# Optimization experiments

Measured on AMD Instinct MI355X. Metric: run time of the kernel, lower is better.

## Reference

```python
import jax, jax.numpy as jnp
import numpy as np

B, S, T = 64, 64, 64          # batch, encoder seq len, decoder context_length
V, D, H, L = 32000, 512, 1024, 256  # vocab, embed, hidden, latent


def _gru_cell(x, h, W_ih, W_hh, b_ih, b_hh):
    # PyTorch GRUCell math. x:[B,D_in], h:[B,H]
    gi = x @ W_ih.T + b_ih            # [B,3H]
    gh = h @ W_hh.T + b_hh            # [B,3H]
    i_r, i_z, i_n = jnp.split(gi, 3, axis=-1)
    h_r, h_z, h_n = jnp.split(gh, 3, axis=-1)
    r = jax.nn.sigmoid(i_r + h_r)
    z = jax.nn.sigmoid(i_z + h_z)
    n = jnp.tanh(i_n + r * h_n)
    return (1.0 - z) * n + z * h


def setup_inputs() -> dict:
    key = jax.random.key(0)
    ks = jax.random.split(key, 16)
    s = 0.02
    inp = {
        "x": jax.random.randint(ks[0], (B, S), 0, V),
        "eps": jax.random.normal(ks[1], (B, L), dtype=jnp.float32),
        "E": jax.random.normal(ks[2], (V, D), dtype=jnp.float32) * s,
        # encoder GRU
        "W_ih_enc": jax.random.normal(ks[3], (3 * H, D), dtype=jnp.float32) * s,
        "W_hh_enc": jax.random.normal(ks[4], (3 * H, H), dtype=jnp.float32) * s,
        "b_ih_enc": jnp.zeros((3 * H,), jnp.float32),
        "b_hh_enc": jnp.zeros((3 * H,), jnp.float32),
        # latent heads
        "W_mu": jax.random.normal(ks[5], (L, H), dtype=jnp.float32) * s,
        "b_mu": jnp.zeros((L,), jnp.float32),
        "W_lv": jax.random.normal(ks[6], (L, H), dtype=jnp.float32) * s,
        "b_lv": jnp.zeros((L,), jnp.float32),
        # decoder proj_h: latent -> hidden
        "W_proj": jax.random.normal(ks[7], (H, L), dtype=jnp.float32) * s,
        "b_proj": jnp.zeros((H,), jnp.float32),
        # decoder GRU cell
        "W_ih_dec": jax.random.normal(ks[8], (3 * H, D), dtype=jnp.float32) * s,
        "W_hh_dec": jax.random.normal(ks[9], (3 * H, H), dtype=jnp.float32) * s,
        "b_ih_dec": jnp.zeros((3 * H,), jnp.float32),
        "b_hh_dec": jnp.zeros((3 * H,), jnp.float32),
        # output projection hidden -> vocab
        "W_out": jax.random.normal(ks[10], (V, H), dtype=jnp.float32) * s,
        "b_out": jnp.zeros((V,), jnp.float32),
    }
    return inp


def reference(x, eps, E, W_ih_enc, W_hh_enc, b_ih_enc, b_hh_enc,
              W_mu, b_mu, W_lv, b_lv, W_proj, b_proj,
              W_ih_dec, W_hh_dec, b_ih_dec, b_hh_dec, W_out, b_out):
    # --- encode ---
    xe = E[x]                                  # [B,S,D]
    h0 = jnp.zeros((x.shape[0], H), xe.dtype)

    def enc_step(h, xt):
        h = _gru_cell(xt, h, W_ih_enc, W_hh_enc, b_ih_enc, b_hh_enc)
        return h, None

    h_last, _ = jax.lax.scan(enc_step, h0, jnp.swapaxes(xe, 0, 1))  # scan over S
    mu = h_last @ W_mu.T + b_mu                # [B,L]
    logvar = h_last @ W_lv.T + b_lv            # [B,L]

    # --- reparametrize ---
    z = mu + eps * jnp.exp(0.5 * logvar)       # [B,L]

    h_dec0 = z @ W_proj.T + b_proj             # [B,H]
    x0 = jnp.zeros((x.shape[0], D), xe.dtype)  # step 0 input is None -> zeros

    def dec_step(carry, _):
        h, xin = carry
        h = _gru_cell(xin, h, W_ih_dec, W_hh_dec, b_ih_dec, b_hh_dec)
        logits = h @ W_out.T + b_out           # [B,V]
        nxt = jnp.argmax(logits, axis=-1)      # [B]
        return (h, E[nxt]), logits

    _, logits_seq = jax.lax.scan(dec_step, (h_dec0, x0), None, length=T)
    outputs = jnp.swapaxes(logits_seq, 0, 1)   # [B,T,V]
    return outputs, mu, logvar
```

## Files before the change

### kernel.cpp

```cpp
#include <hip/hip_runtime.h>

#define B_ 64
#define S_ 64
#define T_ 64
#define V_ 32000
#define D_ 512
#define H_ 1024
#define L_ 256

typedef _Float16 f16;
typedef __attribute__((ext_vector_type(4))) _Float16 f16x4;
typedef __attribute__((ext_vector_type(8))) _Float16 f16x8;
typedef __attribute__((ext_vector_type(16))) float f32x16;

#define INV2048 (1.0f / 2048.0f)

__device__ __forceinline__ void write_frag(f16* __restrict__ Aohi, f16* __restrict__ Aolo,
                                           int b, int j, float hv) {
  const f16 hi = (f16)hv;
  const f16 lo = (f16)((hv - (float)hi) * 2048.0f);
  const long long fo =
      (((long long)(b >> 5) * 64 + (j >> 4)) * 64 + ((b & 31) + 32 * ((j >> 3) & 1))) * 8 + (j & 7);
  Aohi[fo] = hi;
  Aolo[fo] = lo;
}

template <int K>
__global__ __launch_bounds__(256) void k_pack_wf(
    const float* __restrict__ W, f16* __restrict__ Bhi, f16* __restrict__ Blo)
{
  const int n = blockIdx.x;
  const int k = threadIdx.x * 4;
  if (k >= K) return;
  float4 w = *reinterpret_cast<const float4*>(W + (long long)n * K + k);
  float wv[4] = {w.x, w.y, w.z, w.w};
  f16x4 hi, lo;
#pragma unroll
  for (int i = 0; i < 4; ++i) {
    const f16 h = (f16)wv[i];
    hi[i] = h;
    lo[i] = (f16)((wv[i] - (float)h) * 2048.0f);
  }
  const int nt = n >> 5;
  const int lane = (n & 31) + 32 * ((k >> 3) & 1);
  const int ks = k >> 4;
  const long long off = (((long long)nt * (K / 16) + ks) * 64 + lane) * 8 + (k & 7);
  *reinterpret_cast<f16x4*>(Bhi + off) = hi;
  *reinterpret_cast<f16x4*>(Blo + off) = lo;
}

__global__ __launch_bounds__(128) void k_pack_xe(
    const int* __restrict__ x, const float* __restrict__ E,
    f16* __restrict__ XAhi, f16* __restrict__ XAlo)
{
  const int m = blockIdx.x;
  const int s = m >> 6, b = m & 63;
  const int k = threadIdx.x * 4;
  const long long tok = x[b * S_ + s];
  float4 w = *reinterpret_cast<const float4*>(E + tok * D_ + k);
  float wv[4] = {w.x, w.y, w.z, w.w};
  f16x4 hi, lo;
#pragma unroll
  for (int i = 0; i < 4; ++i) {
    const f16 h = (f16)wv[i];
    hi[i] = h;
    lo[i] = (f16)((wv[i] - (float)h) * 2048.0f);
  }
  const int mt = m >> 5;
  const int lane = (m & 31) + 32 * ((k >> 3) & 1);
  const int ks = k >> 4;
  const long long off = (((long long)mt * 32 + ks) * 64 + lane) * 8 + (k & 7);
  *reinterpret_cast<f16x4*>(XAhi + off) = hi;
  *reinterpret_cast<f16x4*>(XAlo + off) = lo;
}

__global__ __launch_bounds__(256) void k_gates_mfma(
    const f16* __restrict__ XAhi, const f16* __restrict__ XAlo,
    const f16* __restrict__ Bhi, const f16* __restrict__ Blo,
    const float* __restrict__ b_ih, float* __restrict__ Gi)
{
  __shared__ float cand[4][64][33];
  const int tid = threadIdx.x;
  const int lane = tid & 63;
  const int wv = __builtin_amdgcn_readfirstlane(tid >> 6);
  const int s = blockIdx.x / 24;
  const int ng = blockIdx.x % 24;
  const int nt = ng * 4 + wv;

  f32x16 aM0, aM1, aLa0, aLa1, aLb0, aLb1;
#pragma unroll
  for (int i = 0; i < 16; ++i) {
    aM0[i] = 0.f; aM1[i] = 0.f; aLa0[i] = 0.f; aLa1[i] = 0.f; aLb0[i] = 0.f; aLb1[i] = 0.f;
  }

  const f16x8* pB_h = reinterpret_cast<const f16x8*>(Bhi) + ((long long)nt * 32) * 64 + lane;
  const f16x8* pB_l = reinterpret_cast<const f16x8*>(Blo) + ((long long)nt * 32) * 64 + lane;
  const f16x8* pA_h = reinterpret_cast<const f16x8*>(XAhi) + ((long long)s * 64) * 64 + lane;
  const f16x8* pA_l = reinterpret_cast<const f16x8*>(XAlo) + ((long long)s * 64) * 64 + lane;

#pragma unroll 4
  for (int ks = 0; ks < 32; ++ks) {
    const int o = ks * 64;
    f16x8 bh = pB_h[o];
    f16x8 bl = pB_l[o];
    f16x8 a0 = pA_h[o];
    f16x8 a1 = pA_h[o + 32 * 64];
    f16x8 l0 = pA_l[o];
    f16x8 l1 = pA_l[o + 32 * 64];
    aM0 = __builtin_amdgcn_mfma_f32_32x32x16_f16(a0, bh, aM0, 0, 0, 0);
    aM1 = __builtin_amdgcn_mfma_f32_32x32x16_f16(a1, bh, aM1, 0, 0, 0);
    aLa0 = __builtin_amdgcn_mfma_f32_32x32x16_f16(a0, bl, aLa0, 0, 0, 0);
    aLa1 = __builtin_amdgcn_mfma_f32_32x32x16_f16(a1, bl, aLa1, 0, 0, 0);
    aLb0 = __builtin_amdgcn_mfma_f32_32x32x16_f16(l0, bh, aLb0, 0, 0, 0);
    aLb1 = __builtin_amdgcn_mfma_f32_32x32x16_f16(l1, bh, aLb1, 0, 0, 0);
  }

  {
    const int l = lane & 31;
    const int rbase = 4 * (lane >> 5);
#pragma unroll
    for (int reg = 0; reg < 16; ++reg) {
      const int row = (reg & 3) + 8 * (reg >> 2) + rbase;
      cand[wv][row][l] = aM0[reg] + (aLa0[reg] + aLb0[reg]) * INV2048;
      cand[wv][row + 32][l] = aM1[reg] + (aLa1[reg] + aLb1[reg]) * INV2048;
    }
  }
  __syncthreads();
  const int bn0 = ng * 128;
#pragma unroll
  for (int i = 0; i < 8; ++i) {
    const int idx = i * 256 + tid;
    const int b4 = (idx & 15) * 4;
    const int nl = idx >> 4;
    const float bi = b_ih[bn0 + nl];
    float4 o;
    o.x = cand[nl >> 5][b4 + 0][nl & 31] + bi;
    o.y = cand[nl >> 5][b4 + 1][nl & 31] + bi;
    o.z = cand[nl >> 5][b4 + 2][nl & 31] + bi;
    o.w = cand[nl >> 5][b4 + 3][nl & 31] + bi;
    *reinterpret_cast<float4*>(&Gi[((long long)s * (3 * H_) + bn0 + nl) * 64 + b4]) = o;
  }
}

__global__ __launch_bounds__(256) void k_hh_mfma(
    const f16* __restrict__ Ahi, const f16* __restrict__ Alo,
    const f16* __restrict__ Bhi, const f16* __restrict__ Blo,
    float* __restrict__ preH)
{
  __shared__ float cand[4][64][33];
  const int tid = threadIdx.x;
  const int lane = tid & 63;
  const int wv = __builtin_amdgcn_readfirstlane(tid >> 6);
  const int nt = blockIdx.x;

  f32x16 aM0, aM1, aLa0, aLa1, aLb0, aLb1;
#pragma unroll
  for (int i = 0; i < 16; ++i) {
    aM0[i] = 0.f; aM1[i] = 0.f; aLa0[i] = 0.f; aLa1[i] = 0.f; aLb0[i] = 0.f; aLb1[i] = 0.f;
  }

  const f16x8* pB_h = reinterpret_cast<const f16x8*>(Bhi) + ((long long)nt * 64 + wv * 16) * 64 + lane;
  const f16x8* pB_l = reinterpret_cast<const f16x8*>(Blo) + ((long long)nt * 64 + wv * 16) * 64 + lane;
  const f16x8* pA_h = reinterpret_cast<const f16x8*>(Ahi) + (long long)(wv * 16) * 64 + lane;
  const f16x8* pA_l = reinterpret_cast<const f16x8*>(Alo) + (long long)(wv * 16) * 64 + lane;

#pragma unroll 4
  for (int q = 0; q < 16; ++q) {
    const int o = q * 64;
    f16x8 bh = pB_h[o];
    f16x8 bl = pB_l[o];
    f16x8 a0 = pA_h[o];
    f16x8 a1 = pA_h[o + 4096];
    f16x8 l0 = pA_l[o];
    f16x8 l1 = pA_l[o + 4096];
    aM0 = __builtin_amdgcn_mfma_f32_32x32x16_f16(a0, bh, aM0, 0, 0, 0);
    aM1 = __builtin_amdgcn_mfma_f32_32x32x16_f16(a1, bh, aM1, 0, 0, 0);
    aLa0 = __builtin_amdgcn_mfma_f32_32x32x16_f16(a0, bl, aLa0, 0, 0, 0);
    aLa1 = __builtin_amdgcn_mfma_f32_32x32x16_f16(a1, bl, aLa1, 0, 0, 0);
    aLb0 = __builtin_amdgcn_mfma_f32_32x32x16_f16(l0, bh, aLb0, 0, 0, 0);
    aLb1 = __builtin_amdgcn_mfma_f32_32x32x16_f16(l1, bh, aLb1, 0, 0, 0);
  }

  {
    const int l = lane & 31;
    const int rbase = 4 * (lane >> 5);
#pragma unroll
    for (int reg = 0; reg < 16; ++reg) {
      const int row = (reg & 3) + 8 * (reg >> 2) + rbase;
      cand[wv][row][l] = aM0[reg] + (aLa0[reg] + aLb0[reg]) * INV2048;
      cand[wv][row + 32][l] = aM1[reg] + (aLa1[reg] + aLb1[reg]) * INV2048;
    }
  }
  __syncthreads();
#pragma unroll
  for (int i = 0; i < 8; ++i) {
    const int idx = i * 256 + tid;
    const int b = idx & 63;
    const int l = idx >> 6;
    const float v = cand[0][b][l] + cand[1][b][l] + cand[2][b][l] + cand[3][b][l];
    preH[((long long)nt * 32 + l) * 64 + b] = v;
  }
}

__global__ __launch_bounds__(256) void k_apply_enc(
    const float* __restrict__ preH, const float* __restrict__ Gi_t,
    const float* __restrict__ b_hh,
    const float* __restrict__ hT_in, float* __restrict__ hT_out,
    f16* __restrict__ Aohi, f16* __restrict__ Aolo)
{
  const int idx = blockIdx.x * 256 + threadIdx.x;
  const int b = idx & 63;
  const int j = idx >> 6;
  const float gr = preH[(long long)j * 64 + b] + Gi_t[(long long)j * 64 + b] + b_hh[j];
  const float gz = preH[(long long)(H_ + j) * 64 + b] + Gi_t[(long long)(H_ + j) * 64 + b] + b_hh[H_ + j];
  const float gin = Gi_t[(long long)(2 * H_ + j) * 64 + b];
  const float ghn = preH[(long long)(2 * H_ + j) * 64 + b] + b_hh[2 * H_ + j];
  const float r = 1.f / (1.f + expf(-gr));
  const float z = 1.f / (1.f + expf(-gz));
  const float n = tanhf(fmaf(r, ghn, gin));
  const float hp = hT_in[(long long)j * 64 + b];
  const float hv = (1.f - z) * n + z * hp;
  hT_out[(long long)j * 64 + b] = hv;
  write_frag(Aohi, Aolo, b, j, hv);
}

template <int XMODE>
__global__ __launch_bounds__(1024) void k_dec_apply(
    const float* __restrict__ E, const unsigned long long* __restrict__ bp,
    const float* __restrict__ W_ih,
    const float* __restrict__ b_ih, const float* __restrict__ b_hh,
    const float* __restrict__ preH, const float* __restrict__ hT_in,
    float* __restrict__ hT_out, f16* __restrict__ Aohi, f16* __restrict__ Aolo)
{
  __shared__ float4 a_lds[64 * 64];
  __shared__ float red[12 * 3 * 64];
  __shared__ int toks[64];
  const int tid = threadIdx.x;
  const int lane = tid & 63;
  const int wv = __builtin_amdgcn_readfirstlane(tid >> 6);
  const int jj = wv & 3;
  const int ks = wv >> 2;
  const int j = blockIdx.x * 4 + jj;
  const int kf16 = tid & 63;
  const int msub = tid >> 6;

  float accR = 0.f, accZ = 0.f, accIN = 0.f;

  if constexpr (XMODE == 2) {
#pragma unroll
    for (int rr = 0; rr < 4; ++rr) {
      const int r = wv + rr * 16;
      unsigned long long kk = 0ull;
#pragma unroll
      for (int i = 0; i < 8; ++i) {
        const unsigned long long q = bp[(long long)r * 512 + lane + i * 64];
        if (q > kk) kk = q;
      }
#pragma unroll
      for (int m = 1; m < 64; m <<= 1) {
        const unsigned long long q = __shfl_xor(kk, m, 64);
        if (q > kk) kk = q;
      }
      if (lane == 0) toks[r] = (int)(0xFFFFFFFFu - (unsigned)(kk & 0xFFFFFFFFull));
    }
    __syncthreads();

    const float* wr = W_ih + (long long)j * D_;
    const float* wz = W_ih + (long long)(j + H_) * D_;
    const float* wn = W_ih + (long long)(j + 2 * H_) * D_;
    for (int c = 0; c < 2; ++c) {
      __syncthreads();
#pragma unroll
      for (int p = 0; p < 4; ++p) {
        const int m = p * 16 + msub;
        const long long tok = toks[m];
        float4 v = *reinterpret_cast<const float4*>(E + tok * D_ + c * 256 + kf16 * 4);
        a_lds[m * 64 + (kf16 ^ (m & 7))] = v;
      }
      __syncthreads();
#pragma unroll 4
      for (int q = 0; q < 16; ++q) {
        const int kf = ks * 16 + q;
        float4 a = a_lds[lane * 64 + (kf ^ (lane & 7))];
        float4 w0 = *reinterpret_cast<const float4*>(wr + c * 256 + kf * 4);
        float4 w1 = *reinterpret_cast<const float4*>(wz + c * 256 + kf * 4);
        float4 w2 = *reinterpret_cast<const float4*>(wn + c * 256 + kf * 4);
        accR = fmaf(w0.x, a.x, accR); accR = fmaf(w0.y, a.y, accR);
        accR = fmaf(w0.z, a.z, accR); accR = fmaf(w0.w, a.w, accR);
        accZ = fmaf(w1.x, a.x, accZ); accZ = fmaf(w1.y, a.y, accZ);
        accZ = fmaf(w1.z, a.z, accZ); accZ = fmaf(w1.w, a.w, accZ);
        accIN = fmaf(w2.x, a.x, accIN); accIN = fmaf(w2.y, a.y, accIN);
        accIN = fmaf(w2.z, a.z, accIN); accIN = fmaf(w2.w, a.w, accIN);
      }
    }
  }

  if (ks > 0) {
    float* rp = red + (((ks - 1) * 4 + jj) * 3) * 64 + lane;
    rp[0] = accR; rp[64] = accZ; rp[128] = accIN;
  }
  __syncthreads();
  if (ks == 0) {
#pragma unroll
    for (int t2 = 0; t2 < 3; ++t2) {
      const float* rp = red + ((t2 * 4 + jj) * 3) * 64 + lane;
      accR += rp[0]; accZ += rp[64]; accIN += rp[128];
    }
    const float gr = accR + preH[(long long)j * 64 + lane] + b_ih[j] + b_hh[j];
    const float gz = accZ + preH[(long long)(H_ + j) * 64 + lane] + b_ih[H_ + j] + b_hh[H_ + j];
    const float gin = accIN + b_ih[2 * H_ + j];
    const float ghn = preH[(long long)(2 * H_ + j) * 64 + lane] + b_hh[2 * H_ + j];
    const float r = 1.f / (1.f + expf(-gr));
    const float z = 1.f / (1.f + expf(-gz));
    const float n = tanhf(fmaf(r, ghn, gin));
    const float hp = hT_in[(long long)j * 64 + lane];
    const float hv = (1.f - z) * n + z * hp;
    hT_out[(long long)j * 64 + lane] = hv;
    write_frag(Aohi, Aolo, lane, j, hv);
  }
}

__global__ __launch_bounds__(256) void k_logits_hh(
    const f16* __restrict__ Ahi, const f16* __restrict__ Alo,
    const f16* __restrict__ WOhi, const f16* __restrict__ WOlo,
    const f16* __restrict__ WHhi, const f16* __restrict__ WHlo,
    const float* __restrict__ b_out, float* __restrict__ out,
    unsigned long long* __restrict__ bestPart, float* __restrict__ preH, int t)
{
  __shared__ float cand[4][64][33];
  __shared__ unsigned long long wbest[4][64];
  const int tid = threadIdx.x;
  const int lane = tid & 63;
  const int wv = __builtin_amdgcn_readfirstlane(tid >> 6);

  if (blockIdx.x >= 500) {
    const int hhb = blockIdx.x - 500;
    const int nt = hhb * 4 + wv;
    f32x16 aM0, aM1, aLa0, aLa1, aLb0, aLb1;
#pragma unroll
    for (int i = 0; i < 16; ++i) {
      aM0[i] = 0.f; aM1[i] = 0.f; aLa0[i] = 0.f; aLa1[i] = 0.f; aLb0[i] = 0.f; aLb1[i] = 0.f;
    }
    const f16x8* pB_h = reinterpret_cast<const f16x8*>(WHhi) + ((long long)nt * 64) * 64 + lane;
    const f16x8* pB_l = reinterpret_cast<const f16x8*>(WHlo) + ((long long)nt * 64) * 64 + lane;
    const f16x8* pA_h = reinterpret_cast<const f16x8*>(Ahi) + lane;
    const f16x8* pA_l = reinterpret_cast<const f16x8*>(Alo) + lane;
#pragma unroll 4
    for (int ksi = 0; ksi < 64; ++ksi) {
      const int o = ksi * 64;
      f16x8 bh = pB_h[o];
      f16x8 bl = pB_l[o];
      f16x8 a0 = pA_h[o];
      f16x8 a1 = pA_h[o + 4096];
      f16x8 l0 = pA_l[o];
      f16x8 l1 = pA_l[o + 4096];
      aM0 = __builtin_amdgcn_mfma_f32_32x32x16_f16(a0, bh, aM0, 0, 0, 0);
      aM1 = __builtin_amdgcn_mfma_f32_32x32x16_f16(a1, bh, aM1, 0, 0, 0);
      aLa0 = __builtin_amdgcn_mfma_f32_32x32x16_f16(a0, bl, aLa0, 0, 0, 0);
      aLa1 = __builtin_amdgcn_mfma_f32_32x32x16_f16(a1, bl, aLa1, 0, 0, 0);
      aLb0 = __builtin_amdgcn_mfma_f32_32x32x16_f16(l0, bh, aLb0, 0, 0, 0);
      aLb1 = __builtin_amdgcn_mfma_f32_32x32x16_f16(l1, bh, aLb1, 0, 0, 0);
    }
    {
      const int l = lane & 31;
      const int rbase = 4 * (lane >> 5);
#pragma unroll
      for (int reg = 0; reg < 16; ++reg) {
        const int row = (reg & 3) + 8 * (reg >> 2) + rbase;
        cand[wv][row][l] = aM0[reg] + (aLa0[reg] + aLb0[reg]) * INV2048;
        cand[wv][row + 32][l] = aM1[reg] + (aLa1[reg] + aLb1[reg]) * INV2048;
      }
    }
    __syncthreads();
#pragma unroll
    for (int i = 0; i < 8; ++i) {
      const int idx = i * 256 + tid;
      const int b4 = (idx & 15) * 4;
      const int nl = idx >> 4;
      float4 o;
      o.x = cand[nl >> 5][b4 + 0][nl & 31];
      o.y = cand[nl >> 5][b4 + 1][nl & 31];
      o.z = cand[nl >> 5][b4 + 2][nl & 31];
      o.w = cand[nl >> 5][b4 + 3][nl & 31];
      *reinterpret_cast<float4*>(&preH[((long long)hhb * 128 + nl) * 64 + b4]) = o;
    }
    return;
  }

  const int p = wv >> 1;
  const int kh = wv & 1;
  const int nt = blockIdx.x * 2 + p;

  f32x16 accM0, accM1, accL0, accL1;
#pragma unroll
  for (int i = 0; i < 16; ++i) { accM0[i] = 0.f; accM1[i] = 0.f; accL0[i] = 0.f; accL1[i] = 0.f; }

  const int kb = kh * 32 * 64;
  const f16x8* pAh0 = reinterpret_cast<const f16x8*>(Ahi) + kb + lane;
  const f16x8* pAh1 = reinterpret_cast<const f16x8*>(Ahi) + 4096 + kb + lane;
  const f16x8* pAl0 = reinterpret_cast<const f16x8*>(Alo) + kb + lane;
  const f16x8* pAl1 = reinterpret_cast<const f16x8*>(Alo) + 4096 + kb + lane;
  const f16x8* pBh = reinterpret_cast<const f16x8*>(WOhi) + (long long)nt * 4096 + kb + lane;
  const f16x8* pBl = reinterpret_cast<const f16x8*>(WOlo) + (long long)nt * 4096 + kb + lane;

#pragma unroll 4
  for (int ksi = 0; ksi < 32; ++ksi) {
    const int o = ksi * 64;
    f16x8 bh = pBh[o];
    f16x8 bl = pBl[o];
    f16x8 ah0 = pAh0[o];
    f16x8 ah1 = pAh1[o];
    f16x8 al0 = pAl0[o];
    f16x8 al1 = pAl1[o];
    accM0 = __builtin_amdgcn_mfma_f32_32x32x16_f16(ah0, bh, accM0, 0, 0, 0);
    accM1 = __builtin_amdgcn_mfma_f32_32x32x16_f16(ah1, bh, accM1, 0, 0, 0);
    accL0 = __builtin_amdgcn_mfma_f32_32x32x16_f16(ah0, bl, accL0, 0, 0, 0);
    accL1 = __builtin_amdgcn_mfma_f32_32x32x16_f16(ah1, bl, accL1, 0, 0, 0);
    accL0 = __builtin_amdgcn_mfma_f32_32x32x16_f16(al0, bh, accL0, 0, 0, 0);
    accL1 = __builtin_amdgcn_mfma_f32_32x32x16_f16(al1, bh, accL1, 0, 0, 0);
  }

  const int l31 = lane & 31;
  const int rbase = 4 * (lane >> 5);

  if (kh == 1) {
#pragma unroll
    for (int reg = 0; reg < 16; ++reg) {
      const int row0 = (reg & 3) + 8 * (reg >> 2) + rbase;
      cand[2 + p][row0][l31] = accM0[reg] + accL0[reg] * INV2048;
      cand[2 + p][row0 + 32][l31] = accM1[reg] + accL1[reg] * INV2048;
    }
  }
  __syncthreads();
  if (kh == 0) {
    const int nn = nt * 32 + l31;
    const float bo = b_out[nn];
#pragma unroll
    for (int reg = 0; reg < 16; ++reg) {
      const int row0 = (reg & 3) + 8 * (reg >> 2) + rbase;
      const float v0 = accM0[reg] + accL0[reg] * INV2048 + cand[2 + p][row0][l31] + bo;
      __builtin_nontemporal_store(v0, &out[(long long)row0 * (T_ * (long long)V_) + (long long)t * V_ + nn]);
      const int row1 = row0 + 32;
      const float v1 = accM1[reg] + accL1[reg] * INV2048 + cand[2 + p][row1][l31] + bo;
      __builtin_nontemporal_store(v1, &out[(long long)row1 * (T_ * (long long)V_) + (long long)t * V_ + nn]);
      cand[2 + p][row0][l31] = v0;
      cand[2 + p][row1][l31] = v1;
    }
  }
  __syncthreads();
  {
    const int w = tid >> 6;
    const int s = w & 1;
    const int r = tid & 63;
    const int nb = (blockIdx.x * 2 + s) * 32;
    unsigned long long kk = 0ull;
#pragma unroll
    for (int l0 = 0; l0 < 32; ++l0) {
      const int l = (l0 + r) & 31;
      const float v = cand[2 + s][r][l];
      unsigned u = __float_as_uint(v);
      u = (u & 0x80000000u) ? ~u : (u | 0x80000000u);
      const unsigned long long key = ((unsigned long long)u << 32) |
          (unsigned long long)(0xFFFFFFFFu - (unsigned)(nb + l));
      if (key > kk) kk = key;
    }
    wbest[w][r] = kk;
  }
  __syncthreads();
  if (tid < 64) {
    unsigned long long kk = wbest[0][tid];
#pragma unroll
    for (int w = 1; w < 4; ++w) { const unsigned long long q = wbest[w][tid]; if (q > kk) kk = q; }
    bestPart[(long long)tid * 512 + blockIdx.x] = kk;
  }
}

__global__ __launch_bounds__(256) void k_mu_lv_z(
    const float* __restrict__ hT, const float* __restrict__ W_mu, const float* __restrict__ b_mu,
    const float* __restrict__ W_lv, const float* __restrict__ b_lv,
    const float* __restrict__ eps, float* __restrict__ out_mu, float* __restrict__ out_lv,
    float* __restrict__ zT)
{
  const int lane = threadIdx.x & 63;
  const int wv = __builtin_amdgcn_readfirstlane(threadIdx.x >> 6);
  const int l = blockIdx.x * 4 + wv;
  const float* wm = W_mu + (long long)l * H_;
  const float* wl = W_lv + (long long)l * H_;
  float am = 0.f, av = 0.f;
#pragma unroll 8
  for (int k = 0; k < H_; ++k) {
    const float h = hT[k * 64 + lane];
    am = fmaf(wm[k], h, am);
    av = fmaf(wl[k], h, av);
  }
  const float mu = am + b_mu[l];
  const float lv = av + b_lv[l];
  out_mu[lane * L_ + l] = mu;
  out_lv[lane * L_ + l] = lv;
  zT[l * 64 + lane] = fmaf(eps[lane * L_ + l], expf(0.5f * lv), mu);
}

__global__ __launch_bounds__(256) void k_proj(
    const float* __restrict__ zT, const float* __restrict__ W_proj,
    const float* __restrict__ b_proj, float* __restrict__ hT0,
    f16* __restrict__ Aohi, f16* __restrict__ Aolo)
{
  const int lane = threadIdx.x & 63;
  const int wv = __builtin_amdgcn_readfirstlane(threadIdx.x >> 6);
  const int j = blockIdx.x * 4 + wv;
  const float* wr = W_proj + (long long)j * L_;
  float acc = 0.f;
#pragma unroll 8
  for (int k = 0; k < L_; ++k) acc = fmaf(wr[k], zT[k * 64 + lane], acc);
  const float hv = acc + b_proj[j];
  hT0[(long long)j * 64 + lane] = hv;
  write_frag(Aohi, Aolo, lane, j, hv);
}

extern "C" void kernel_launch(void* const* d_in, const int* in_sizes, int n_in,
                              void* d_out, int out_size, void* d_ws, size_t ws_size,
                              hipStream_t stream) {
  (void)in_sizes; (void)n_in; (void)out_size;
  const int*   x        = (const int*)d_in[0];
  const float* eps      = (const float*)d_in[1];
  const float* E        = (const float*)d_in[2];
  const float* W_ih_enc = (const float*)d_in[3];
  const float* W_hh_enc = (const float*)d_in[4];
  const float* b_ih_enc = (const float*)d_in[5];
  const float* b_hh_enc = (const float*)d_in[6];
  const float* W_mu     = (const float*)d_in[7];
  const float* b_mu     = (const float*)d_in[8];
  const float* W_lv     = (const float*)d_in[9];
  const float* b_lv     = (const float*)d_in[10];
  const float* W_proj   = (const float*)d_in[11];
  const float* b_proj   = (const float*)d_in[12];
  const float* W_ih_dec = (const float*)d_in[13];
  const float* W_hh_dec = (const float*)d_in[14];
  const float* b_ih_dec = (const float*)d_in[15];
  const float* b_hh_dec = (const float*)d_in[16];
  const float* W_out    = (const float*)d_in[17];
  const float* b_out    = (const float*)d_in[18];

  float* out = (float*)d_out;
  const long long OFF_MU = (long long)B_ * T_ * V_;
  const long long OFF_LV = OFF_MU + (long long)B_ * L_;

  float* ws = (float*)d_ws;
  float* hA   = ws + 0;
  float* dA   = ws + 65536;
  float* zT   = ws + 131072;
  unsigned long long* bestPart = (unsigned long long*)(ws + 147456);
  float* preH = ws + 212992;
  f16* frAhi  = (f16*)(ws + 409600);
  f16* frAlo  = (f16*)(ws + 442368);
  f16* WHEhi  = (f16*)(ws + 475136);
  f16* WHElo  = (f16*)(ws + 2048000);
  f16* WHDhi  = (f16*)(ws + 3620864);
  f16* WHDlo  = (f16*)(ws + 5193728);
  f16* WIEhi  = (f16*)(ws + 6766592);
  f16* WIElo  = (f16*)(ws + 7553024);
  f16* XAhi   = (f16*)(ws + 8339456);
  f16* XAlo   = (f16*)(ws + 9388032);
  float* Gi   = ws + 10436608;
  f16* WOhi   = (f16*)(ws + 8339456);
  f16* WOlo   = (f16*)(ws + 24723456);
  const size_t WS_NEED = (size_t)41107456 * 4;
  if (ws_size < WS_NEED) return;

  hipMemsetAsync(hA, 0, (size_t)H_ * B_ * sizeof(float), stream);
  hipMemsetAsync(frAhi, 0, (size_t)2 * 65536 * sizeof(f16), stream);
  hipMemsetAsync(bestPart, 0, (size_t)64 * 512 * 8, stream);

  k_pack_wf<1024><<<3 * H_, 256, 0, stream>>>(W_hh_enc, WHEhi, WHElo);
  k_pack_wf<1024><<<3 * H_, 256, 0, stream>>>(W_hh_dec, WHDhi, WHDlo);
  k_pack_wf<512><<<3 * H_, 128, 0, stream>>>(W_ih_enc, WIEhi, WIElo);
  k_pack_xe<<<S_ * B_, 128, 0, stream>>>(x, E, XAhi, XAlo);

  k_gates_mfma<<<64 * 24, 256, 0, stream>>>(XAhi, XAlo, WIEhi, WIElo, b_ih_enc, Gi);

  for (int t = 0; t < S_; ++t) {
    k_hh_mfma<<<96, 256, 0, stream>>>(frAhi, frAlo, WHEhi, WHElo, preH);
    k_apply_enc<<<256, 256, 0, stream>>>(preH, Gi + (long long)t * 3 * H_ * B_,
                                         b_hh_enc, hA, hA, frAhi, frAlo);
  }

  k_mu_lv_z<<<64, 256, 0, stream>>>(hA, W_mu, b_mu, W_lv, b_lv, eps,
                                    out + OFF_MU, out + OFF_LV, zT);
  k_proj<<<256, 256, 0, stream>>>(zT, W_proj, b_proj, dA, frAhi, frAlo);

  k_pack_wf<1024><<<V_, 256, 0, stream>>>(W_out, WOhi, WOlo);

  k_hh_mfma<<<96, 256, 0, stream>>>(frAhi, frAlo, WHDhi, WHDlo, preH);

  for (int t = 0; t < T_; ++t) {
    if (t == 0) {
      k_dec_apply<0><<<256, 1024, 0, stream>>>(
          E, nullptr, W_ih_dec, b_ih_dec, b_hh_dec, preH, dA, dA, frAhi, frAlo);
    } else {
      k_dec_apply<2><<<256, 1024, 0, stream>>>(
          E, bestPart, W_ih_dec, b_ih_dec, b_hh_dec, preH, dA, dA, frAhi, frAlo);
    }
    k_logits_hh<<<524, 256, 0, stream>>>(frAhi, frAlo, WOhi, WOlo, WHDhi, WHDlo,
                                         b_out, out, bestPart, preH, t);
  }
}
```

Before: 6.257 ms.

## Persistent 256-block logits/hh kernel with uniform K-split tiles and merged low accumulators

The decoder logits+hidden kernel becomes a persistent grid of 256 blocks looping over 1096 uniform work units. Each unit is a 32-wide vocab or hidden tile whose K dimension is split across the four waves and reduced through shared memory. This replaces the old mix of 500 two-tile logits blocks and 24 heavier hh blocks. The partial-argmax buffer grows to 1024 slots per row, with matching changes to the reader and the workspace offsets. Separately, the two low-order correction MFMA streams now accumulate into one register set in all GEMM kernels, freeing registers at the cost of a longer dependent MFMA chain.

```diff
diff --git a/kernel.cpp b/kernel.cpp
--- a/kernel.cpp
+++ b/kernel.cpp
@@ -87,11 +87,9 @@
   const int ng = blockIdx.x % 24;
   const int nt = ng * 4 + wv;
 
-  f32x16 aM0, aM1, aLa0, aLa1, aLb0, aLb1;
-#pragma unroll
-  for (int i = 0; i < 16; ++i) {
-    aM0[i] = 0.f; aM1[i] = 0.f; aLa0[i] = 0.f; aLa1[i] = 0.f; aLb0[i] = 0.f; aLb1[i] = 0.f;
-  }
+  f32x16 aM0, aM1, aL0, aL1;
+#pragma unroll
+  for (int i = 0; i < 16; ++i) { aM0[i] = 0.f; aM1[i] = 0.f; aL0[i] = 0.f; aL1[i] = 0.f; }
 
   const f16x8* pB_h = reinterpret_cast<const f16x8*>(Bhi) + ((long long)nt * 32) * 64 + lane;
   const f16x8* pB_l = reinterpret_cast<const f16x8*>(Blo) + ((long long)nt * 32) * 64 + lane;
@@ -109,10 +107,10 @@
     f16x8 l1 = pA_l[o + 32 * 64];
     aM0 = __builtin_amdgcn_mfma_f32_32x32x16_f16(a0, bh, aM0, 0, 0, 0);
     aM1 = __builtin_amdgcn_mfma_f32_32x32x16_f16(a1, bh, aM1, 0, 0, 0);
-    aLa0 = __builtin_amdgcn_mfma_f32_32x32x16_f16(a0, bl, aLa0, 0, 0, 0);
-    aLa1 = __builtin_amdgcn_mfma_f32_32x32x16_f16(a1, bl, aLa1, 0, 0, 0);
-    aLb0 = __builtin_amdgcn_mfma_f32_32x32x16_f16(l0, bh, aLb0, 0, 0, 0);
-    aLb1 = __builtin_amdgcn_mfma_f32_32x32x16_f16(l1, bh, aLb1, 0, 0, 0);
+    aL0 = __builtin_amdgcn_mfma_f32_32x32x16_f16(a0, bl, aL0, 0, 0, 0);
+    aL0 = __builtin_amdgcn_mfma_f32_32x32x16_f16(l0, bh, aL0, 0, 0, 0);
+    aL1 = __builtin_amdgcn_mfma_f32_32x32x16_f16(a1, bl, aL1, 0, 0, 0);
+    aL1 = __builtin_amdgcn_mfma_f32_32x32x16_f16(l1, bh, aL1, 0, 0, 0);
   }
 
   {
@@ -121,8 +119,8 @@
 #pragma unroll
     for (int reg = 0; reg < 16; ++reg) {
       const int row = (reg & 3) + 8 * (reg >> 2) + rbase;
-      cand[wv][row][l] = aM0[reg] + (aLa0[reg] + aLb0[reg]) * INV2048;
-      cand[wv][row + 32][l] = aM1[reg] + (aLa1[reg] + aLb1[reg]) * INV2048;
+      cand[wv][row][l] = aM0[reg] + aL0[reg] * INV2048;
+      cand[wv][row + 32][l] = aM1[reg] + aL1[reg] * INV2048;
     }
   }
   __syncthreads();
@@ -153,11 +151,9 @@
   const int wv = __builtin_amdgcn_readfirstlane(tid >> 6);
   const int nt = blockIdx.x;
 
-  f32x16 aM0, aM1, aLa0, aLa1, aLb0, aLb1;
-#pragma unroll
-  for (int i = 0; i < 16; ++i) {
-    aM0[i] = 0.f; aM1[i] = 0.f; aLa0[i] = 0.f; aLa1[i] = 0.f; aLb0[i] = 0.f; aLb1[i] = 0.f;
-  }
+  f32x16 aM0, aM1, aL0, aL1;
+#pragma unroll
+  for (int i = 0; i < 16; ++i) { aM0[i] = 0.f; aM1[i] = 0.f; aL0[i] = 0.f; aL1[i] = 0.f; }
 
   const f16x8* pB_h = reinterpret_cast<const f16x8*>(Bhi) + ((long long)nt * 64 + wv * 16) * 64 + lane;
   const f16x8* pB_l = reinterpret_cast<const f16x8*>(Blo) + ((long long)nt * 64 + wv * 16) * 64 + lane;
@@ -175,10 +171,10 @@
     f16x8 l1 = pA_l[o + 4096];
     aM0 = __builtin_amdgcn_mfma_f32_32x32x16_f16(a0, bh, aM0, 0, 0, 0);
     aM1 = __builtin_amdgcn_mfma_f32_32x32x16_f16(a1, bh, aM1, 0, 0, 0);
-    aLa0 = __builtin_amdgcn_mfma_f32_32x32x16_f16(a0, bl, aLa0, 0, 0, 0);
-    aLa1 = __builtin_amdgcn_mfma_f32_32x32x16_f16(a1, bl, aLa1, 0, 0, 0);
-    aLb0 = __builtin_amdgcn_mfma_f32_32x32x16_f16(l0, bh, aLb0, 0, 0, 0);
-    aLb1 = __builtin_amdgcn_mfma_f32_32x32x16_f16(l1, bh, aLb1, 0, 0, 0);
+    aL0 = __builtin_amdgcn_mfma_f32_32x32x16_f16(a0, bl, aL0, 0, 0, 0);
+    aL0 = __builtin_amdgcn_mfma_f32_32x32x16_f16(l0, bh, aL0, 0, 0, 0);
+    aL1 = __builtin_amdgcn_mfma_f32_32x32x16_f16(a1, bl, aL1, 0, 0, 0);
+    aL1 = __builtin_amdgcn_mfma_f32_32x32x16_f16(l1, bh, aL1, 0, 0, 0);
   }
 
   {
@@ -187,8 +183,8 @@
 #pragma unroll
     for (int reg = 0; reg < 16; ++reg) {
       const int row = (reg & 3) + 8 * (reg >> 2) + rbase;
-      cand[wv][row][l] = aM0[reg] + (aLa0[reg] + aLb0[reg]) * INV2048;
-      cand[wv][row + 32][l] = aM1[reg] + (aLa1[reg] + aLb1[reg]) * INV2048;
+      cand[wv][row][l] = aM0[reg] + aL0[reg] * INV2048;
+      cand[wv][row + 32][l] = aM1[reg] + aL1[reg] * INV2048;
     }
   }
   __syncthreads();
@@ -252,8 +248,8 @@
       const int r = wv + rr * 16;
       unsigned long long kk = 0ull;
 #pragma unroll
-      for (int i = 0; i < 8; ++i) {
-        const unsigned long long q = bp[(long long)r * 512 + lane + i * 64];
+      for (int i = 0; i < 16; ++i) {
+        const unsigned long long q = bp[(long long)r * 1024 + lane + i * 64];
         if (q > kk) kk = q;
       }
 #pragma unroll
@@ -332,146 +328,95 @@
   const int tid = threadIdx.x;
   const int lane = tid & 63;
   const int wv = __builtin_amdgcn_readfirstlane(tid >> 6);
-
-  if (blockIdx.x >= 500) {
-    const int hhb = blockIdx.x - 500;
-    const int nt = hhb * 4 + wv;
-    f32x16 aM0, aM1, aLa0, aLa1, aLb0, aLb1;
-#pragma unroll
-    for (int i = 0; i < 16; ++i) {
-      aM0[i] = 0.f; aM1[i] = 0.f; aLa0[i] = 0.f; aLa1[i] = 0.f; aLb0[i] = 0.f; aLb1[i] = 0.f;
-    }
-    const f16x8* pB_h = reinterpret_cast<const f16x8*>(WHhi) + ((long long)nt * 64) * 64 + lane;
-    const f16x8* pB_l = reinterpret_cast<const f16x8*>(WHlo) + ((long long)nt * 64) * 64 + lane;
-    const f16x8* pA_h = reinterpret_cast<const f16x8*>(Ahi) + lane;
-    const f16x8* pA_l = reinterpret_cast<const f16x8*>(Alo) + lane;
-#pragma unroll 4
-    for (int ksi = 0; ksi < 64; ++ksi) {
-      const int o = ksi * 64;
-      f16x8 bh = pB_h[o];
-      f16x8 bl = pB_l[o];
-      f16x8 a0 = pA_h[o];
-      f16x8 a1 = pA_h[o + 4096];
-      f16x8 l0 = pA_l[o];
-      f16x8 l1 = pA_l[o + 4096];
+  const int kb = wv * 16 * 64;
+  const int l31 = lane & 31;
+  const int rbase = 4 * (lane >> 5);
+
+  for (int u = blockIdx.x; u < 1096; u += 256) {
+    f32x16 aM0, aM1, aL0, aL1;
+#pragma unroll
+    for (int i = 0; i < 16; ++i) { aM0[i] = 0.f; aM1[i] = 0.f; aL0[i] = 0.f; aL1[i] = 0.f; }
+
+    const bool isLog = (u < 1000);
+    const int nt = isLog ? u : (u - 1000);
+    const f16x8* pBh = reinterpret_cast<const f16x8*>(isLog ? WOhi : WHhi) + (long long)nt * 4096 + kb + lane;
+    const f16x8* pBl = reinterpret_cast<const f16x8*>(isLog ? WOlo : WHlo) + (long long)nt * 4096 + kb + lane;
+    const f16x8* pAh = reinterpret_cast<const f16x8*>(Ahi) + kb + lane;
+    const f16x8* pAl = reinterpret_cast<const f16x8*>(Alo) + kb + lane;
+
+#pragma unroll 8
+    for (int q = 0; q < 16; ++q) {
+      const int o = q * 64;
+      f16x8 bh = pBh[o];
+      f16x8 bl = pBl[o];
+      f16x8 a0 = pAh[o];
+      f16x8 a1 = pAh[o + 4096];
+      f16x8 l0 = pAl[o];
+      f16x8 l1 = pAl[o + 4096];
       aM0 = __builtin_amdgcn_mfma_f32_32x32x16_f16(a0, bh, aM0, 0, 0, 0);
       aM1 = __builtin_amdgcn_mfma_f32_32x32x16_f16(a1, bh, aM1, 0, 0, 0);
-      aLa0 = __builtin_amdgcn_mfma_f32_32x32x16_f16(a0, bl, aLa0, 0, 0, 0);
-      aLa1 = __builtin_amdgcn_mfma_f32_32x32x16_f16(a1, bl, aLa1, 0, 0, 0);
-      aLb0 = __builtin_amdgcn_mfma_f32_32x32x16_f16(l0, bh, aLb0, 0, 0, 0);
-      aLb1 = __builtin_amdgcn_mfma_f32_32x32x16_f16(l1, bh, aLb1, 0, 0, 0);
-    }
-    {
-      const int l = lane & 31;
-      const int rbase = 4 * (lane >> 5);
-#pragma unroll
-      for (int reg = 0; reg < 16; ++reg) {
-        const int row = (reg & 3) + 8 * (reg >> 2) + rbase;
-        cand[wv][row][l] = aM0[reg] + (aLa0[reg] + aLb0[reg]) * INV2048;
-        cand[wv][row + 32][l] = aM1[reg] + (aLa1[reg] + aLb1[reg]) * INV2048;
-      }
+      aL0 = __builtin_amdgcn_mfma_f32_32x32x16_f16(a0, bl, aL0, 0, 0, 0);
+      aL0 = __builtin_amdgcn_mfma_f32_32x32x16_f16(l0, bh, aL0, 0, 0, 0);
+      aL1 = __builtin_amdgcn_mfma_f32_32x32x16_f16(a1, bl, aL1, 0, 0, 0);
+      aL1 = __builtin_amdgcn_mfma_f32_32x32x16_f16(l1, bh, aL1, 0, 0, 0);
+    }
+
+#pragma unroll
+    for (int reg = 0; reg < 16; ++reg) {
+      const int row = (reg & 3) + 8 * (reg >> 2) + rbase;
+      cand[wv][row][l31] = aM0[reg] + aL0[reg] * INV2048;
+      cand[wv][row + 32][l31] = aM1[reg] + aL1[reg] * INV2048;
     }
     __syncthreads();
-#pragma unroll
-    for (int i = 0; i < 8; ++i) {
-      const int idx = i * 256 + tid;
-      const int b4 = (idx & 15) * 4;
-      const int nl = idx >> 4;
-      float4 o;
-      o.x = cand[nl >> 5][b4 + 0][nl & 31];
-      o.y = cand[nl >> 5][b4 + 1][nl & 31];
-      o.z = cand[nl >> 5][b4 + 2][nl & 31];
-      o.w = cand[nl >> 5][b4 + 3][nl & 31];
-      *reinterpret_cast<float4*>(&preH[((long long)hhb * 128 + nl) * 64 + b4]) = o;
-    }
-    return;
-  }
-
-  const int p = wv >> 1;
-  const int kh = wv & 1;
-  const int nt = blockIdx.x * 2 + p;
-
-  f32x16 accM0, accM1, accL0, accL1;
-#pragma unroll
-  for (int i = 0; i < 16; ++i) { accM0[i] = 0.f; accM1[i] = 0.f; accL0[i] = 0.f; accL1[i] = 0.f; }
-
-  const int kb = kh * 32 * 64;
-  const f16x8* pAh0 = reinterpret_cast<const f16x8*>(Ahi) + kb + lane;
-  const f16x8* pAh1 = reinterpret_cast<const f16x8*>(Ahi) + 4096 + kb + lane;
-  const f16x8* pAl0 = reinterpret_cast<const f16x8*>(Alo) + kb + lane;
-  const f16x8* pAl1 = reinterpret_cast<const f16x8*>(Alo) + 4096 + kb + lane;
-  const f16x8* pBh = reinterpret_cast<const f16x8*>(WOhi) + (long long)nt * 4096 + kb + lane;
-  const f16x8* pBl = reinterpret_cast<const f16x8*>(WOlo) + (long long)nt * 4096 + kb + lane;
-
-#pragma unroll 4
-  for (int ksi = 0; ksi < 32; ++ksi) {
-    const int o = ksi * 64;
-    f16x8 bh = pBh[o];
-    f16x8 bl = pBl[o];
-    f16x8 ah0 = pAh0[o];
-    f16x8 ah1 = pAh1[o];
-    f16x8 al0 = pAl0[o];
-    f16x8 al1 = pAl1[o];
-    accM0 = __builtin_amdgcn_mfma_f32_32x32x16_f16(ah0, bh, accM0, 0, 0, 0);
-    accM1 = __builtin_amdgcn_mfma_f32_32x32x16_f16(ah1, bh, accM1, 0, 0, 0);
-    accL0 = __builtin_amdgcn_mfma_f32_32x32x16_f16(ah0, bl, accL0, 0, 0, 0);
-    accL1 = __builtin_amdgcn_mfma_f32_32x32x16_f16(ah1, bl, accL1, 0, 0, 0);
-    accL0 = __builtin_amdgcn_mfma_f32_32x32x16_f16(al0, bh, accL0, 0, 0, 0);
-    accL1 = __builtin_amdgcn_mfma_f32_32x32x16_f16(al1, bh, accL1, 0, 0, 0);
-  }
-
-  const int l31 = lane & 31;
-  const int rbase = 4 * (lane >> 5);
-
-  if (kh == 1) {
-#pragma unroll
-    for (int reg = 0; reg < 16; ++reg) {
-      const int row0 = (reg & 3) + 8 * (reg >> 2) + rbase;
-      cand[2 + p][row0][l31] = accM0[reg] + accL0[reg] * INV2048;
-      cand[2 + p][row0 + 32][l31] = accM1[reg] + accL1[reg] * INV2048;
-    }
-  }
-  __syncthreads();
-  if (kh == 0) {
-    const int nn = nt * 32 + l31;
-    const float bo = b_out[nn];
-#pragma unroll
-    for (int reg = 0; reg < 16; ++reg) {
-      const int row0 = (reg & 3) + 8 * (reg >> 2) + rbase;
-      const float v0 = accM0[reg] + accL0[reg] * INV2048 + cand[2 + p][row0][l31] + bo;
-      __builtin_nontemporal_store(v0, &out[(long long)row0 * (T_ * (long long)V_) + (long long)t * V_ + nn]);
-      const int row1 = row0 + 32;
-      const float v1 = accM1[reg] + accL1[reg] * INV2048 + cand[2 + p][row1][l31] + bo;
-      __builtin_nontemporal_store(v1, &out[(long long)row1 * (T_ * (long long)V_) + (long long)t * V_ + nn]);
-      cand[2 + p][row0][l31] = v0;
-      cand[2 + p][row1][l31] = v1;
-    }
-  }
-  __syncthreads();
-  {
-    const int w = tid >> 6;
-    const int s = w & 1;
-    const int r = tid & 63;
-    const int nb = (blockIdx.x * 2 + s) * 32;
-    unsigned long long kk = 0ull;
-#pragma unroll
-    for (int l0 = 0; l0 < 32; ++l0) {
-      const int l = (l0 + r) & 31;
-      const float v = cand[2 + s][r][l];
-      unsigned u = __float_as_uint(v);
-      u = (u & 0x80000000u) ? ~u : (u | 0x80000000u);
-      const unsigned long long key = ((unsigned long long)u << 32) |
-          (unsigned long long)(0xFFFFFFFFu - (unsigned)(nb + l));
-      if (key > kk) kk = key;
-    }
-    wbest[w][r] = kk;
-  }
-  __syncthreads();
-  if (tid < 64) {
-    unsigned long long kk = wbest[0][tid];
-#pragma unroll
-    for (int w = 1; w < 4; ++w) { const unsigned long long q = wbest[w][tid]; if (q > kk) kk = q; }
-    bestPart[(long long)tid * 512 + blockIdx.x] = kk;
+
+    if (isLog) {
+#pragma unroll
+      for (int i = 0; i < 8; ++i) {
+        const int idx = i * 256 + tid;
+        const int col = idx & 31;
+        const int row = idx >> 5;
+        const int nn = nt * 32 + col;
+        const float v = cand[0][row][col] + cand[1][row][col] + cand[2][row][col] +
+                        cand[3][row][col] + b_out[nn];
+        __builtin_nontemporal_store(v, &out[(long long)row * (T_ * (long long)V_) + (long long)t * V_ + nn]);
+        cand[0][row][col] = v;
+      }
+      __syncthreads();
+      {
+        const int r = tid & 63;
+        const int q = tid >> 6;
+        unsigned long long kk = 0ull;
+#pragma unroll
+        for (int cc = 0; cc < 8; ++cc) {
+          const int col = q * 8 + cc;
+          const float v = cand[0][r][col];
+          unsigned uu = __float_as_uint(v);
+          uu = (uu & 0x80000000u) ? ~uu : (uu | 0x80000000u);
+          const unsigned long long key = ((unsigned long long)uu << 32) |
+              (unsigned long long)(0xFFFFFFFFu - (unsigned)(nt * 32 + col));
+          if (key > kk) kk = key;
+        }
+        wbest[q][r] = kk;
+      }
+      __syncthreads();
+      if (tid < 64) {
+        unsigned long long kk = wbest[0][tid];
+#pragma unroll
+        for (int w = 1; w < 4; ++w) { const unsigned long long q = wbest[w][tid]; if (q > kk) kk = q; }
+        bestPart[(long long)tid * 1024 + u] = kk;
+      }
+      __syncthreads();
+    } else {
+#pragma unroll
+      for (int i = 0; i < 8; ++i) {
+        const int idx = i * 256 + tid;
+        const int b = idx & 63;
+        const int l = idx >> 6;
+        const float v = cand[0][b][l] + cand[1][b][l] + cand[2][b][l] + cand[3][b][l];
+        preH[((long long)nt * 32 + l) * 64 + b] = v;
+      }
+      __syncthreads();
+    }
   }
 }
 
@@ -550,26 +495,26 @@
   float* dA   = ws + 65536;
   float* zT   = ws + 131072;
   unsigned long long* bestPart = (unsigned long long*)(ws + 147456);
-  float* preH = ws + 212992;
-  f16* frAhi  = (f16*)(ws + 409600);
-  f16* frAlo  = (f16*)(ws + 442368);
-  f16* WHEhi  = (f16*)(ws + 475136);
-  f16* WHElo  = (f16*)(ws + 2048000);
-  f16* WHDhi  = (f16*)(ws + 3620864);
-  f16* WHDlo  = (f16*)(ws + 5193728);
-  f16* WIEhi  = (f16*)(ws + 6766592);
-  f16* WIElo  = (f16*)(ws + 7553024);
-  f16* XAhi   = (f16*)(ws + 8339456);
-  f16* XAlo   = (f16*)(ws + 9388032);
-  float* Gi   = ws + 10436608;
-  f16* WOhi   = (f16*)(ws + 8339456);
-  f16* WOlo   = (f16*)(ws + 24723456);
-  const size_t WS_NEED = (size_t)41107456 * 4;
+  float* preH = ws + 278528;
+  f16* frAhi  = (f16*)(ws + 475136);
+  f16* frAlo  = (f16*)(ws + 507904);
+  f16* WHEhi  = (f16*)(ws + 540672);
+  f16* WHElo  = (f16*)(ws + 2113536);
+  f16* WHDhi  = (f16*)(ws + 3686400);
+  f16* WHDlo  = (f16*)(ws + 5259264);
+  f16* WIEhi  = (f16*)(ws + 6832128);
+  f16* WIElo  = (f16*)(ws + 7618560);
+  f16* XAhi   = (f16*)(ws + 8404992);
+  f16* XAlo   = (f16*)(ws + 9453568);
+  float* Gi   = ws + 10502144;
+  f16* WOhi   = (f16*)(ws + 8404992);
+  f16* WOlo   = (f16*)(ws + 24788992);
+  const size_t WS_NEED = (size_t)41172992 * 4;
   if (ws_size < WS_NEED) return;
 
   hipMemsetAsync(hA, 0, (size_t)H_ * B_ * sizeof(float), stream);
   hipMemsetAsync(frAhi, 0, (size_t)2 * 65536 * sizeof(f16), stream);
-  hipMemsetAsync(bestPart, 0, (size_t)64 * 512 * 8, stream);
+  hipMemsetAsync(bestPart, 0, (size_t)64 * 1024 * 8, stream);
 
   k_pack_wf<1024><<<3 * H_, 256, 0, stream>>>(W_hh_enc, WHEhi, WHElo);
   k_pack_wf<1024><<<3 * H_, 256, 0, stream>>>(W_hh_dec, WHDhi, WHDlo);
@@ -600,7 +545,7 @@
       k_dec_apply<2><<<256, 1024, 0, stream>>>(
           E, bestPart, W_ih_dec, b_ih_dec, b_hh_dec, preH, dA, dA, frAhi, frAlo);
     }
-    k_logits_hh<<<524, 256, 0, stream>>>(frAhi, frAlo, WOhi, WOlo, WHDhi, WHDlo,
+    k_logits_hh<<<256, 256, 0, stream>>>(frAhi, frAlo, WOhi, WOlo, WHDhi, WHDlo,
                                          b_out, out, bestPart, preH, t);
   }
 }
```

Result: faster. 5.755 ms (-8.0%).
